# Optimization experiments

Hardware: AMD Instinct MI355X
Metric: run time of the kernel (lower is better)

Reference implementation:

```python
import jax, jax.numpy as jnp
import numpy as np

N, E, IN, H, OUT, K = 50000, 800000, 128, 64, 64, 1024


def setup_inputs() -> dict:
    key = jax.random.key(0)
    ks = jax.random.split(key, 8)
    x = jax.random.normal(ks[0], (N, IN), dtype=jnp.float32)
    edge_index = jax.random.randint(ks[1], (2, E), 0, N, dtype=jnp.int32)
    cluster_id = jax.random.randint(ks[2], (N,), 0, K, dtype=jnp.int32)
    W1 = jax.random.normal(ks[3], (IN, H), dtype=jnp.float32) / np.float32(np.sqrt(IN))
    b1 = jnp.zeros((H,), jnp.float32)
    W2 = jax.random.normal(ks[4], (H, OUT), dtype=jnp.float32) / np.float32(np.sqrt(H))
    b2 = jnp.zeros((OUT,), jnp.float32)
    W_skip = jax.random.normal(ks[5], (H, OUT), dtype=jnp.float32) / np.float32(np.sqrt(H))
    b_skip = jnp.zeros((OUT,), jnp.float32)
    alpha = jnp.full((1,), 1.5, jnp.float32)
    return dict(x=x, edge_index=edge_index, cluster_id=cluster_id, W1=W1, b1=b1,
                W2=W2, b2=b2, W_skip=W_skip, b_skip=b_skip, alpha=alpha)


def gcn_conv_sparse(x, src, dst, n, W, b):
    # PyG GCNConv: transform, then D^{-1/2}(A+I)D^{-1/2} aggregation, then bias.
    h = x @ W  # [n, F_out]
    deg = jax.ops.segment_sum(jnp.ones_like(src, dtype=h.dtype), dst, num_segments=n) + 1.0
    dinv = jax.lax.rsqrt(deg)
    norm = dinv[src] * dinv[dst]  # [E]
    agg = jax.ops.segment_sum(h[src] * norm[:, None], dst, num_segments=n)
    agg = agg + (dinv * dinv)[:, None] * h  # self-loop term
    return agg + b


def reference(x, edge_index, cluster_id, W1, b1, W2, b2, W_skip, b_skip, alpha):
    src, dst = edge_index[0], edge_index[1]
    # conv1 + ReLU (dropout is identity in eval mode)
    x1 = jax.nn.relu(gcn_conv_sparse(x, src, dst, N, W1, b1))  # [N, H]

    # pool_by_partition: scatter-mean node features into K clusters
    sums = jax.ops.segment_sum(x1, cluster_id, num_segments=K)  # [K, H]
    counts = jnp.maximum(jax.ops.segment_sum(jnp.ones((N,), x1.dtype), cluster_id, num_segments=K), 1.0)
    x_p = sums / counts[:, None]

    # deduped pooled edges, self-loops removed == dense 0/1 adjacency with zero diag (K small)
    cu, cv = cluster_id[src], cluster_id[dst]
    A = jnp.zeros((K, K), x1.dtype).at[cu, cv].set(1.0)
    A = A * (1.0 - jnp.eye(K, dtype=x1.dtype))
    A_hat = A + jnp.eye(K, dtype=x1.dtype)
    deg_p = jnp.sum(A_hat, axis=0)  # in-degree at target (PyG computes deg on col)
    dinv_p = jax.lax.rsqrt(deg_p)
    A_norm = dinv_p[:, None] * A_hat * dinv_p[None, :]  # [src, dst]
    h_p = x_p @ W2
    x_p2 = jnp.einsum('st,sf->tf', A_norm, h_p) + b2  # [K, OUT]

    # gather-broadcast + strengthened skip head
    up = x_p2[cluster_id]  # [N, OUT]
    skip = x1 @ W_skip + b_skip
    logits = up + jax.nn.relu(alpha)[0] * skip
    return logits
```

## Files before the change

kernel.cpp:

```cpp
#include <hip/hip_runtime.h>

#define NN 50000
#define NE 800000
#define FIN 128
#define FH 64
#define FOUT 64
#define KC 1024
#define CAP 64
#define EPB 2048
#define NCH ((NE + EPB - 1) / EPB)
#define NBK ((NN + 255) / 256)
#define BCAP 4608

typedef unsigned char  u8;
typedef unsigned short u16;
typedef unsigned int   u32;


__global__ __launch_bounds__(256) void k_part(const int* __restrict__ src,
                                              const int* __restrict__ dst,
                                              const int* __restrict__ cid,
                                              int* __restrict__ gcur,
                                              u32* __restrict__ bin,
                                              u8* __restrict__ AT) {
    __shared__ int hist[256], off[256], cur[256], gbase[256];
    __shared__ u32 sorted[EPB];
    int t = threadIdx.x;
    hist[t] = 0; cur[t] = 0;
    __syncthreads();
    int e0 = blockIdx.x * EPB, e1 = min(NE, e0 + EPB);
    for (int e = e0 + t; e < e1; e += 256)
        atomicAdd(&hist[dst[e] >> 8], 1);
    __syncthreads();
    int v = hist[t];
    off[t] = v;
    __syncthreads();
    for (int o = 1; o < 256; o <<= 1) {
        int u = (t >= o) ? off[t - o] : 0;
        __syncthreads();
        off[t] += u;
        __syncthreads();
    }
    int ex = off[t] - v;
    __syncthreads();
    off[t] = ex;
    __syncthreads();
    for (int e = e0 + t; e < e1; e += 256) {
        int d = dst[e], s = src[e];
        int b = d >> 8, local = d & 255;
        int cu = cid[s], cv = cid[d];
        if (cu != cv) AT[(size_t)cv * KC + cu] = 1;
        int p = off[b] + atomicAdd(&cur[b], 1);
        sorted[p] = ((u32)b << 24) | ((u32)local << 16) | (u32)s;
    }
    __syncthreads();
    if (t < NBK && hist[t]) gbase[t] = atomicAdd(&gcur[t], hist[t]);
    __syncthreads();
    int cnt = e1 - e0;
    for (int i = t; i < cnt; i += 256) {
        u32 e = sorted[i];
        int b = e >> 24;
        int idx = gbase[b] + (i - off[b]);
        if (idx < BCAP) bin[(size_t)b * BCAP + idx] = e;
    }
}

__global__ __launch_bounds__(256) void k_slots(const int* __restrict__ gcur,
                                               const u32* __restrict__ bin,
                                               const int* __restrict__ cid,
                                               int* __restrict__ deg,
                                               float* __restrict__ dinv,
                                               int* __restrict__ counts,
                                               u16* __restrict__ slots) {
    __shared__ u16 sbuf[256 * CAP];
    __shared__ int c_lds[256];
    int t = threadIdx.x, b = blockIdx.x;
    c_lds[t] = 0;
    __syncthreads();
    int cnt = min(gcur[b], BCAP);
    const u32* bp = bin + (size_t)b * BCAP;
    for (int i = t; i < cnt; i += 256) {
        u32 e = bp[i];
        int local = (e >> 16) & 255;
        int pos = atomicAdd(&c_lds[local], 1);
        if (pos < CAP) sbuf[local * CAP + pos] = (u16)(e & 0xffffu);
    }
    __syncthreads();
    int node = b * 256 + t;
    if (node < NN) {
        int d = c_lds[t];
        deg[node] = d;
        dinv[node] = rsqrtf((float)d + 1.0f);
        atomicAdd(&counts[cid[node]], 1);
    }
    int rows = min(256, NN - b * 256);
    int n4 = rows * (CAP * 2 / 16);
    const uint4* sb4 = (const uint4*)sbuf;
    uint4* gs4 = (uint4*)(slots + (size_t)b * 256 * CAP);
    for (int j = t; j < n4; j += 256) gs4[j] = sb4[j];
}

__global__ __launch_bounds__(256) void k_gemm1(const float* __restrict__ x,
                                               const float* __restrict__ W1,
                                               const float* __restrict__ dinv,
                                               float* __restrict__ h) {
    __shared__ float Ws[FIN * FH];
    __shared__ float Xs[32 * FIN];
    int t = threadIdx.x;
    int row_base = blockIdx.x * 32;
    for (int i = t; i < FIN * FH; i += 256) Ws[i] = W1[i];
    {
        const float4* x4 = (const float4*)x;
        float4* xs4 = (float4*)Xs;
        for (int i = t; i < 32 * 32; i += 256) {
            int r = i >> 5, k4 = i & 31;
            int row = row_base + r;
            float4 v = make_float4(0.f, 0.f, 0.f, 0.f);
            if (row < NN) v = x4[(size_t)row * 32 + k4];
            xs4[i] = v;
        }
    }
    __syncthreads();
    int col = t & 31, grp = t >> 5;
    int r0 = grp * 4;
    const float4* p0 = (const float4*)&Xs[(r0 + 0) * FIN];
    const float4* p1 = (const float4*)&Xs[(r0 + 1) * FIN];
    const float4* p2 = (const float4*)&Xs[(r0 + 2) * FIN];
    const float4* p3 = (const float4*)&Xs[(r0 + 3) * FIN];
    float acc00 = 0.f, acc01 = 0.f, acc10 = 0.f, acc11 = 0.f;
    float acc20 = 0.f, acc21 = 0.f, acc30 = 0.f, acc31 = 0.f;
#pragma unroll 2
    for (int k4 = 0; k4 < FIN / 4; ++k4) {
        float4 a0 = p0[k4], a1 = p1[k4], a2 = p2[k4], a3 = p3[k4];
        const float* wp = &Ws[(k4 * 4) * FH + col];
        float w00 = wp[0],          w01 = wp[32];
        float w10 = wp[FH],         w11 = wp[FH + 32];
        float w20 = wp[2 * FH],     w21 = wp[2 * FH + 32];
        float w30 = wp[3 * FH],     w31 = wp[3 * FH + 32];
        acc00 = fmaf(a0.x, w00, fmaf(a0.y, w10, fmaf(a0.z, w20, fmaf(a0.w, w30, acc00))));
        acc01 = fmaf(a0.x, w01, fmaf(a0.y, w11, fmaf(a0.z, w21, fmaf(a0.w, w31, acc01))));
        acc10 = fmaf(a1.x, w00, fmaf(a1.y, w10, fmaf(a1.z, w20, fmaf(a1.w, w30, acc10))));
        acc11 = fmaf(a1.x, w01, fmaf(a1.y, w11, fmaf(a1.z, w21, fmaf(a1.w, w31, acc11))));
        acc20 = fmaf(a2.x, w00, fmaf(a2.y, w10, fmaf(a2.z, w20, fmaf(a2.w, w30, acc20))));
        acc21 = fmaf(a2.x, w01, fmaf(a2.y, w11, fmaf(a2.z, w21, fmaf(a2.w, w31, acc21))));
        acc30 = fmaf(a3.x, w00, fmaf(a3.y, w10, fmaf(a3.z, w20, fmaf(a3.w, w30, acc30))));
        acc31 = fmaf(a3.x, w01, fmaf(a3.y, w11, fmaf(a3.z, w21, fmaf(a3.w, w31, acc31))));
    }
    int row0 = row_base + r0;
    if (row0 + 0 < NN) { float di = dinv[row0 + 0]; h[(size_t)(row0 + 0) * FH + col] = di * acc00; h[(size_t)(row0 + 0) * FH + col + 32] = di * acc01; }
    if (row0 + 1 < NN) { float di = dinv[row0 + 1]; h[(size_t)(row0 + 1) * FH + col] = di * acc10; h[(size_t)(row0 + 1) * FH + col + 32] = di * acc11; }
    if (row0 + 2 < NN) { float di = dinv[row0 + 2]; h[(size_t)(row0 + 2) * FH + col] = di * acc20; h[(size_t)(row0 + 2) * FH + col + 32] = di * acc21; }
    if (row0 + 3 < NN) { float di = dinv[row0 + 3]; h[(size_t)(row0 + 3) * FH + col] = di * acc30; h[(size_t)(row0 + 3) * FH + col + 32] = di * acc31; }
}

__global__ __launch_bounds__(256) void k_gather(const int* __restrict__ deg,
                                                const u16* __restrict__ slots,
                                                const float* __restrict__ dinv,
                                                const float* __restrict__ h,
                                                const float* __restrict__ b1,
                                                const int* __restrict__ cid,
                                                float* __restrict__ x1,
                                                float* __restrict__ sums) {
    int lane = threadIdx.x & 63;
    int node = blockIdx.x * 4 + (threadIdx.x >> 6);
    if (node >= NN) return;
    int q = lane >> 4, fl = lane & 15;
    const float4* h4 = (const float4*)h;
    int cnt = min(deg[node], CAP);
    const u16* cp = slots + (size_t)node * CAP;
    float4 acc = make_float4(0.f, 0.f, 0.f, 0.f);
    {
        int s = (lane < cnt) ? (int)cp[lane] : 0;
        int nFull = cnt >> 2;
        for (int j = 0; j < nFull; ++j) {
            int ss = __shfl(s, j * 4 + q);
            float4 hv = h4[(size_t)ss * 16 + fl];
            acc.x += hv.x; acc.y += hv.y; acc.z += hv.z; acc.w += hv.w;
        }
        int tail = cnt & 3;
        if (tail) {
            int ss = __shfl(s, nFull * 4 + q);
            float m = (q < tail) ? 1.f : 0.f;
            float4 hv = h4[(size_t)ss * 16 + fl];
            acc.x = fmaf(m, hv.x, acc.x);
            acc.y = fmaf(m, hv.y, acc.y);
            acc.z = fmaf(m, hv.z, acc.z);
            acc.w = fmaf(m, hv.w, acc.w);
        }
    }
    acc.x += __shfl_xor(acc.x, 16); acc.y += __shfl_xor(acc.y, 16);
    acc.z += __shfl_xor(acc.z, 16); acc.w += __shfl_xor(acc.w, 16);
    acc.x += __shfl_xor(acc.x, 32); acc.y += __shfl_xor(acc.y, 32);
    acc.z += __shfl_xor(acc.z, 32); acc.w += __shfl_xor(acc.w, 32);
    float di = dinv[node];
    float4 hs = h4[(size_t)node * 16 + fl];
    const float4* b14 = (const float4*)b1;
    float4 bb = b14[fl];
    float4 v;
    v.x = fmaxf(fmaf(di, acc.x + hs.x, bb.x), 0.f);
    v.y = fmaxf(fmaf(di, acc.y + hs.y, bb.y), 0.f);
    v.z = fmaxf(fmaf(di, acc.z + hs.z, bb.z), 0.f);
    v.w = fmaxf(fmaf(di, acc.w + hs.w, bb.w), 0.f);
    if (q == 0) ((float4*)x1)[(size_t)node * 16 + fl] = v;
    int c = cid[node];
    float comp = (q == 0) ? v.x : (q == 1) ? v.y : (q == 2) ? v.z : v.w;
    unsafeAtomicAdd(&sums[(size_t)c * FH + fl * 4 + q], comp);
}

__global__ __launch_bounds__(64) void k_pool(const float* __restrict__ sums,
                                             const int* __restrict__ counts,
                                             const float* __restrict__ W2,
                                             const u8* __restrict__ AT,
                                             float* __restrict__ dinvp,
                                             float* __restrict__ g) {
    __shared__ float xp[FH];
    int s = blockIdx.x, f = threadIdx.x;
    const u32* row = (const u32*)(AT + (size_t)s * KC);
    int pc = __popc(row[f]) + __popc(row[f + 64]) + __popc(row[f + 128]) + __popc(row[f + 192]);
    for (int o = 32; o; o >>= 1) pc += __shfl_xor(pc, o);
    float dp = rsqrtf(1.0f + (float)pc);
    if (f == 0) dinvp[s] = dp;
    float cnt = fmaxf((float)counts[s], 1.0f);
    xp[f] = sums[(size_t)s * FH + f] / cnt;
    __syncthreads();
    float acc = 0.f;
    for (int j = 0; j < FH; ++j) acc = fmaf(xp[j], W2[j * FH + f], acc);
    g[(size_t)s * FH + f] = dp * acc;
}

__global__ __launch_bounds__(256) void k_xp2(const u8* __restrict__ AT,
                                             const float* __restrict__ g,
                                             const float* __restrict__ dinvp,
                                             const float* __restrict__ b2,
                                             float* __restrict__ xp2) {
    __shared__ float4 sm4[4][16];
    int t = blockIdx.x;
    int lane = threadIdx.x & 63, w = threadIdx.x >> 6;
    int q = lane >> 4, fl = lane & 15;
    const u32* roww = (const u32*)(AT + (size_t)t * KC);
    const float4* g4 = (const float4*)g;
    float4 acc = make_float4(0.f, 0.f, 0.f, 0.f);
    int wb = w * 64;
    u32 wv = roww[wb + lane];
    for (int j = 0; j < 16; ++j) {
        u32 word = __shfl((int)wv, j * 4 + q);
        int sidx = (wb + j * 4 + q) * 4;
#pragma unroll
        for (int b = 0; b < 4; ++b) {
            float a = (float)((word >> (8 * b)) & 255u);
            float4 gv = g4[(size_t)(sidx + b) * 16 + fl];
            acc.x = fmaf(a, gv.x, acc.x);
            acc.y = fmaf(a, gv.y, acc.y);
            acc.z = fmaf(a, gv.z, acc.z);
            acc.w = fmaf(a, gv.w, acc.w);
        }
    }
    acc.x += __shfl_xor(acc.x, 16); acc.y += __shfl_xor(acc.y, 16);
    acc.z += __shfl_xor(acc.z, 16); acc.w += __shfl_xor(acc.w, 16);
    acc.x += __shfl_xor(acc.x, 32); acc.y += __shfl_xor(acc.y, 32);
    acc.z += __shfl_xor(acc.z, 32); acc.w += __shfl_xor(acc.w, 32);
    if (q == 0) sm4[w][fl] = acc;
    __syncthreads();
    if (threadIdx.x < 16) {
        int f = threadIdx.x;
        float4 a0 = sm4[0][f], a1 = sm4[1][f], a2 = sm4[2][f], a3 = sm4[3][f];
        float4 gs = g4[(size_t)t * 16 + f];
        float dp = dinvp[t];
        const float4* b24 = (const float4*)b2;
        float4 bb = b24[f];
        float4 o;
        o.x = fmaf(dp, a0.x + a1.x + a2.x + a3.x + gs.x, bb.x);
        o.y = fmaf(dp, a0.y + a1.y + a2.y + a3.y + gs.y, bb.y);
        o.z = fmaf(dp, a0.z + a1.z + a2.z + a3.z + gs.z, bb.z);
        o.w = fmaf(dp, a0.w + a1.w + a2.w + a3.w + gs.w, bb.w);
        ((float4*)xp2)[(size_t)t * 16 + f] = o;
    }
}

__global__ __launch_bounds__(256) void k_final(const float* __restrict__ x1,
                                               const float* __restrict__ Wsk,
                                               const float* __restrict__ bsk,
                                               const float* __restrict__ xp2,
                                               const int* __restrict__ cid,
                                               const float* __restrict__ alpha,
                                               float* __restrict__ out) {
    __shared__ float Ws[FH * FOUT];
    __shared__ float Xs[32 * FH];
    int t = threadIdx.x;
    int row_base = blockIdx.x * 32;
    for (int i = t; i < FH * FOUT; i += 256) Ws[i] = Wsk[i];
    {
        const float4* x4 = (const float4*)x1;
        float4* xs4 = (float4*)Xs;
        for (int i = t; i < 32 * 16; i += 256) {
            int r = i >> 4, k4 = i & 15;
            int row = row_base + r;
            float4 v = make_float4(0.f, 0.f, 0.f, 0.f);
            if (row < NN) v = x4[(size_t)row * 16 + k4];
            xs4[i] = v;
        }
    }
    __syncthreads();
    float al = fmaxf(alpha[0], 0.f);
    int col = t & 31, grp = t >> 5;
    int r0 = grp * 4;
    const float4* p0 = (const float4*)&Xs[(r0 + 0) * FH];
    const float4* p1 = (const float4*)&Xs[(r0 + 1) * FH];
    const float4* p2 = (const float4*)&Xs[(r0 + 2) * FH];
    const float4* p3 = (const float4*)&Xs[(r0 + 3) * FH];
    float acc00 = 0.f, acc01 = 0.f, acc10 = 0.f, acc11 = 0.f;
    float acc20 = 0.f, acc21 = 0.f, acc30 = 0.f, acc31 = 0.f;
#pragma unroll 2
    for (int k4 = 0; k4 < FH / 4; ++k4) {
        float4 a0 = p0[k4], a1 = p1[k4], a2 = p2[k4], a3 = p3[k4];
        const float* wp = &Ws[(k4 * 4) * FOUT + col];
        float w00 = wp[0],           w01 = wp[32];
        float w10 = wp[FOUT],        w11 = wp[FOUT + 32];
        float w20 = wp[2 * FOUT],    w21 = wp[2 * FOUT + 32];
        float w30 = wp[3 * FOUT],    w31 = wp[3 * FOUT + 32];
        acc00 = fmaf(a0.x, w00, fmaf(a0.y, w10, fmaf(a0.z, w20, fmaf(a0.w, w30, acc00))));
        acc01 = fmaf(a0.x, w01, fmaf(a0.y, w11, fmaf(a0.z, w21, fmaf(a0.w, w31, acc01))));
        acc10 = fmaf(a1.x, w00, fmaf(a1.y, w10, fmaf(a1.z, w20, fmaf(a1.w, w30, acc10))));
        acc11 = fmaf(a1.x, w01, fmaf(a1.y, w11, fmaf(a1.z, w21, fmaf(a1.w, w31, acc11))));
        acc20 = fmaf(a2.x, w00, fmaf(a2.y, w10, fmaf(a2.z, w20, fmaf(a2.w, w30, acc20))));
        acc21 = fmaf(a2.x, w01, fmaf(a2.y, w11, fmaf(a2.z, w21, fmaf(a2.w, w31, acc21))));
        acc30 = fmaf(a3.x, w00, fmaf(a3.y, w10, fmaf(a3.z, w20, fmaf(a3.w, w30, acc30))));
        acc31 = fmaf(a3.x, w01, fmaf(a3.y, w11, fmaf(a3.z, w21, fmaf(a3.w, w31, acc31))));
    }
    float bb0 = bsk[col], bb1 = bsk[col + 32];
    int row0 = row_base + r0;
#pragma unroll
    for (int i = 0; i < 4; ++i) {
        float a0 = (i == 0) ? acc00 : (i == 1) ? acc10 : (i == 2) ? acc20 : acc30;
        float a1 = (i == 0) ? acc01 : (i == 1) ? acc11 : (i == 2) ? acc21 : acc31;
        int row = row0 + i;
        if (row < NN) {
            int c = cid[row];
            out[(size_t)row * FOUT + col]      = xp2[(size_t)c * FOUT + col]      + al * (a0 + bb0);
            out[(size_t)row * FOUT + col + 32] = xp2[(size_t)c * FOUT + col + 32] + al * (a1 + bb1);
        }
    }
}

extern "C" void kernel_launch(void* const* d_in, const int* in_sizes, int n_in,
                              void* d_out, int out_size, void* d_ws, size_t ws_size,
                              hipStream_t stream) {
    const float* x    = (const float*)d_in[0];
    const int*   ei   = (const int*)d_in[1];
    const int*   cid  = (const int*)d_in[2];
    const float* W1   = (const float*)d_in[3];
    const float* b1   = (const float*)d_in[4];
    const float* W2   = (const float*)d_in[5];
    const float* b2   = (const float*)d_in[6];
    const float* Wsk  = (const float*)d_in[7];
    const float* bsk  = (const float*)d_in[8];
    const float* alpha= (const float*)d_in[9];
    float* out = (float*)d_out;
    const int* src = ei;
    const int* dst = ei + NE;

    char* ws = (char*)d_ws;
    size_t cur = 0;
    auto alloc = [&](size_t nb) { cur = (cur + 255) & ~(size_t)255; size_t o = cur; cur += nb; return o; };
    size_t o_sums = alloc((size_t)KC * FH * 4);
    size_t o_AT   = alloc((size_t)KC * KC);
    size_t o_cnt  = alloc((size_t)KC * 4);
    size_t o_gcur = alloc((size_t)NBK * 4);
    size_t zero_bytes = cur;
    size_t o_bin  = alloc((size_t)NBK * BCAP * 4);
    size_t o_slot = alloc((size_t)NN * CAP * 2);
    size_t o_deg  = alloc((size_t)NN * 4);
    size_t o_x1   = alloc((size_t)NN * FH * 4);
    size_t o_h    = alloc((size_t)NN * FH * 4);
    size_t o_dinv = alloc((size_t)NN * 4);
    size_t o_g    = alloc((size_t)KC * FH * 4);
    size_t o_xp2  = alloc((size_t)KC * FH * 4);
    size_t o_dinvp= alloc((size_t)KC * 4);
    (void)ws_size; (void)in_sizes; (void)n_in; (void)out_size;

    float* sums = (float*)(ws + o_sums);
    u8*    AT   = (u8*)(ws + o_AT);
    int*   cnt  = (int*)(ws + o_cnt);
    int*   gcur = (int*)(ws + o_gcur);
    u32*   bin  = (u32*)(ws + o_bin);
    u16*   slot = (u16*)(ws + o_slot);
    int*   deg  = (int*)(ws + o_deg);
    float* x1   = (float*)(ws + o_x1);
    float* h    = (float*)(ws + o_h);
    float* dinv = (float*)(ws + o_dinv);
    float* g    = (float*)(ws + o_g);
    float* xp2  = (float*)(ws + o_xp2);
    float* dinvp= (float*)(ws + o_dinvp);

    hipMemsetAsync(d_ws, 0, zero_bytes, stream);

    const int NRB = (NN + 31) / 32;
    k_part  <<<NCH, 256, 0, stream>>>(src, dst, cid, gcur, bin, AT);
    k_slots <<<NBK, 256, 0, stream>>>(gcur, bin, cid, deg, dinv, cnt, slot);
    k_gemm1 <<<NRB, 256, 0, stream>>>(x, W1, dinv, h);
    k_gather<<<(NN + 3) / 4, 256, 0, stream>>>(deg, slot, dinv, h, b1, cid, x1, sums);
    k_pool  <<<KC, 64, 0, stream>>>(sums, cnt, W2, AT, dinvp, g);
    k_xp2   <<<KC, 256, 0, stream>>>(AT, g, dinvp, b2, xp2);
    k_final <<<NRB, 256, 0, stream>>>(x1, Wsk, bsk, xp2, cid, alpha, out);
}
```

Measured before the change: 212.5 us.

## Store intermediate node features in fp16 and cache edges in LDS during partitioning

The transformed features h, written by the first GEMM and gathered per edge, are now stored as half precision, which halves the bytes moved by the random neighbor gather. The GEMM output layout changes so each thread writes adjacent column pairs as half2. Separately, the partition kernel reads each edge's src/dst and cluster ids once, keeps the packed edge in LDS, and reuses it for the local sort instead of reloading from global memory. The fp16 storage adds rounding error to the aggregated features.

```diff
diff --git a/kernel.cpp b/kernel.cpp
--- a/kernel.cpp
+++ b/kernel.cpp
@@ -1,4 +1,5 @@
 #include <hip/hip_runtime.h>
+#include <hip/hip_fp16.h>
 
 #define NN 50000
 #define NE 800000
@@ -16,7 +17,6 @@
 typedef unsigned short u16;
 typedef unsigned int   u32;
 
-
 __global__ __launch_bounds__(256) void k_part(const int* __restrict__ src,
                                               const int* __restrict__ dst,
                                               const int* __restrict__ cid,
@@ -24,13 +24,21 @@
                                               u32* __restrict__ bin,
                                               u8* __restrict__ AT) {
     __shared__ int hist[256], off[256], cur[256], gbase[256];
+    __shared__ u32 raw[EPB];
     __shared__ u32 sorted[EPB];
     int t = threadIdx.x;
     hist[t] = 0; cur[t] = 0;
     __syncthreads();
     int e0 = blockIdx.x * EPB, e1 = min(NE, e0 + EPB);
-    for (int e = e0 + t; e < e1; e += 256)
-        atomicAdd(&hist[dst[e] >> 8], 1);
+    int cnt = e1 - e0;
+    for (int e = e0 + t; e < e1; e += 256) {
+        int d = dst[e], s = src[e];
+        int b = d >> 8, local = d & 255;
+        int cu = cid[s], cv = cid[d];
+        if (cu != cv) AT[(size_t)cv * KC + cu] = 1;
+        atomicAdd(&hist[b], 1);
+        raw[e - e0] = ((u32)b << 24) | ((u32)local << 16) | (u32)s;
+    }
     __syncthreads();
     int v = hist[t];
     off[t] = v;
@@ -45,18 +53,15 @@
     __syncthreads();
     off[t] = ex;
     __syncthreads();
-    for (int e = e0 + t; e < e1; e += 256) {
-        int d = dst[e], s = src[e];
-        int b = d >> 8, local = d & 255;
-        int cu = cid[s], cv = cid[d];
-        if (cu != cv) AT[(size_t)cv * KC + cu] = 1;
+    for (int i = t; i < cnt; i += 256) {
+        u32 e = raw[i];
+        int b = e >> 24;
         int p = off[b] + atomicAdd(&cur[b], 1);
-        sorted[p] = ((u32)b << 24) | ((u32)local << 16) | (u32)s;
+        sorted[p] = e;
     }
     __syncthreads();
     if (t < NBK && hist[t]) gbase[t] = atomicAdd(&gcur[t], hist[t]);
     __syncthreads();
-    int cnt = e1 - e0;
     for (int i = t; i < cnt; i += 256) {
         u32 e = sorted[i];
         int b = e >> 24;
@@ -103,7 +108,7 @@
 __global__ __launch_bounds__(256) void k_gemm1(const float* __restrict__ x,
                                                const float* __restrict__ W1,
                                                const float* __restrict__ dinv,
-                                               float* __restrict__ h) {
+                                               __half* __restrict__ h) {
     __shared__ float Ws[FIN * FH];
     __shared__ float Xs[32 * FIN];
     int t = threadIdx.x;
@@ -121,7 +126,8 @@
         }
     }
     __syncthreads();
-    int col = t & 31, grp = t >> 5;
+    int c = t & 31, grp = t >> 5;
+    int colp = c * 2;
     int r0 = grp * 4;
     const float4* p0 = (const float4*)&Xs[(r0 + 0) * FIN];
     const float4* p1 = (const float4*)&Xs[(r0 + 1) * FIN];
@@ -132,31 +138,32 @@
 #pragma unroll 2
     for (int k4 = 0; k4 < FIN / 4; ++k4) {
         float4 a0 = p0[k4], a1 = p1[k4], a2 = p2[k4], a3 = p3[k4];
-        const float* wp = &Ws[(k4 * 4) * FH + col];
-        float w00 = wp[0],          w01 = wp[32];
-        float w10 = wp[FH],         w11 = wp[FH + 32];
-        float w20 = wp[2 * FH],     w21 = wp[2 * FH + 32];
-        float w30 = wp[3 * FH],     w31 = wp[3 * FH + 32];
-        acc00 = fmaf(a0.x, w00, fmaf(a0.y, w10, fmaf(a0.z, w20, fmaf(a0.w, w30, acc00))));
-        acc01 = fmaf(a0.x, w01, fmaf(a0.y, w11, fmaf(a0.z, w21, fmaf(a0.w, w31, acc01))));
-        acc10 = fmaf(a1.x, w00, fmaf(a1.y, w10, fmaf(a1.z, w20, fmaf(a1.w, w30, acc10))));
-        acc11 = fmaf(a1.x, w01, fmaf(a1.y, w11, fmaf(a1.z, w21, fmaf(a1.w, w31, acc11))));
-        acc20 = fmaf(a2.x, w00, fmaf(a2.y, w10, fmaf(a2.z, w20, fmaf(a2.w, w30, acc20))));
-        acc21 = fmaf(a2.x, w01, fmaf(a2.y, w11, fmaf(a2.z, w21, fmaf(a2.w, w31, acc21))));
-        acc30 = fmaf(a3.x, w00, fmaf(a3.y, w10, fmaf(a3.z, w20, fmaf(a3.w, w30, acc30))));
-        acc31 = fmaf(a3.x, w01, fmaf(a3.y, w11, fmaf(a3.z, w21, fmaf(a3.w, w31, acc31))));
-    }
+        const float* wb = &Ws[(k4 * 4) * FH + colp];
+        float2 w0 = *(const float2*)&wb[0];
+        float2 w1 = *(const float2*)&wb[FH];
+        float2 w2 = *(const float2*)&wb[2 * FH];
+        float2 w3 = *(const float2*)&wb[3 * FH];
+        acc00 = fmaf(a0.x, w0.x, fmaf(a0.y, w1.x, fmaf(a0.z, w2.x, fmaf(a0.w, w3.x, acc00))));
+        acc01 = fmaf(a0.x, w0.y, fmaf(a0.y, w1.y, fmaf(a0.z, w2.y, fmaf(a0.w, w3.y, acc01))));
+        acc10 = fmaf(a1.x, w0.x, fmaf(a1.y, w1.x, fmaf(a1.z, w2.x, fmaf(a1.w, w3.x, acc10))));
+        acc11 = fmaf(a1.x, w0.y, fmaf(a1.y, w1.y, fmaf(a1.z, w2.y, fmaf(a1.w, w3.y, acc11))));
+        acc20 = fmaf(a2.x, w0.x, fmaf(a2.y, w1.x, fmaf(a2.z, w2.x, fmaf(a2.w, w3.x, acc20))));
+        acc21 = fmaf(a2.x, w0.y, fmaf(a2.y, w1.y, fmaf(a2.z, w2.y, fmaf(a2.w, w3.y, acc21))));
+        acc30 = fmaf(a3.x, w0.x, fmaf(a3.y, w1.x, fmaf(a3.z, w2.x, fmaf(a3.w, w3.x, acc30))));
+        acc31 = fmaf(a3.x, w0.y, fmaf(a3.y, w1.y, fmaf(a3.z, w2.y, fmaf(a3.w, w3.y, acc31))));
+    }
+    __half2* h2 = (__half2*)h;
     int row0 = row_base + r0;
-    if (row0 + 0 < NN) { float di = dinv[row0 + 0]; h[(size_t)(row0 + 0) * FH + col] = di * acc00; h[(size_t)(row0 + 0) * FH + col + 32] = di * acc01; }
-    if (row0 + 1 < NN) { float di = dinv[row0 + 1]; h[(size_t)(row0 + 1) * FH + col] = di * acc10; h[(size_t)(row0 + 1) * FH + col + 32] = di * acc11; }
-    if (row0 + 2 < NN) { float di = dinv[row0 + 2]; h[(size_t)(row0 + 2) * FH + col] = di * acc20; h[(size_t)(row0 + 2) * FH + col + 32] = di * acc21; }
-    if (row0 + 3 < NN) { float di = dinv[row0 + 3]; h[(size_t)(row0 + 3) * FH + col] = di * acc30; h[(size_t)(row0 + 3) * FH + col + 32] = di * acc31; }
+    if (row0 + 0 < NN) { float di = dinv[row0 + 0]; h2[(size_t)(row0 + 0) * 32 + c] = __floats2half2_rn(di * acc00, di * acc01); }
+    if (row0 + 1 < NN) { float di = dinv[row0 + 1]; h2[(size_t)(row0 + 1) * 32 + c] = __floats2half2_rn(di * acc10, di * acc11); }
+    if (row0 + 2 < NN) { float di = dinv[row0 + 2]; h2[(size_t)(row0 + 2) * 32 + c] = __floats2half2_rn(di * acc20, di * acc21); }
+    if (row0 + 3 < NN) { float di = dinv[row0 + 3]; h2[(size_t)(row0 + 3) * 32 + c] = __floats2half2_rn(di * acc30, di * acc31); }
 }
 
 __global__ __launch_bounds__(256) void k_gather(const int* __restrict__ deg,
                                                 const u16* __restrict__ slots,
                                                 const float* __restrict__ dinv,
-                                                const float* __restrict__ h,
+                                                const __half* __restrict__ h,
                                                 const float* __restrict__ b1,
                                                 const int* __restrict__ cid,
                                                 float* __restrict__ x1,
@@ -165,7 +172,7 @@
     int node = blockIdx.x * 4 + (threadIdx.x >> 6);
     if (node >= NN) return;
     int q = lane >> 4, fl = lane & 15;
-    const float4* h4 = (const float4*)h;
+    const float2* h2 = (const float2*)h;
     int cnt = min(deg[node], CAP);
     const u16* cp = slots + (size_t)node * CAP;
     float4 acc = make_float4(0.f, 0.f, 0.f, 0.f);
@@ -174,18 +181,22 @@
         int nFull = cnt >> 2;
         for (int j = 0; j < nFull; ++j) {
             int ss = __shfl(s, j * 4 + q);
-            float4 hv = h4[(size_t)ss * 16 + fl];
-            acc.x += hv.x; acc.y += hv.y; acc.z += hv.z; acc.w += hv.w;
+            float2 rawv = h2[(size_t)ss * 16 + fl];
+            float2 f0 = __half22float2(*(__half2*)&rawv.x);
+            float2 f1 = __half22float2(*(__half2*)&rawv.y);
+            acc.x += f0.x; acc.y += f0.y; acc.z += f1.x; acc.w += f1.y;
         }
         int tail = cnt & 3;
         if (tail) {
             int ss = __shfl(s, nFull * 4 + q);
             float m = (q < tail) ? 1.f : 0.f;
-            float4 hv = h4[(size_t)ss * 16 + fl];
-            acc.x = fmaf(m, hv.x, acc.x);
-            acc.y = fmaf(m, hv.y, acc.y);
-            acc.z = fmaf(m, hv.z, acc.z);
-            acc.w = fmaf(m, hv.w, acc.w);
+            float2 rawv = h2[(size_t)ss * 16 + fl];
+            float2 f0 = __half22float2(*(__half2*)&rawv.x);
+            float2 f1 = __half22float2(*(__half2*)&rawv.y);
+            acc.x = fmaf(m, f0.x, acc.x);
+            acc.y = fmaf(m, f0.y, acc.y);
+            acc.z = fmaf(m, f1.x, acc.z);
+            acc.w = fmaf(m, f1.y, acc.w);
         }
     }
     acc.x += __shfl_xor(acc.x, 16); acc.y += __shfl_xor(acc.y, 16);
@@ -193,14 +204,16 @@
     acc.x += __shfl_xor(acc.x, 32); acc.y += __shfl_xor(acc.y, 32);
     acc.z += __shfl_xor(acc.z, 32); acc.w += __shfl_xor(acc.w, 32);
     float di = dinv[node];
-    float4 hs = h4[(size_t)node * 16 + fl];
+    float2 rawv = h2[(size_t)node * 16 + fl];
+    float2 hs0 = __half22float2(*(__half2*)&rawv.x);
+    float2 hs1 = __half22float2(*(__half2*)&rawv.y);
     const float4* b14 = (const float4*)b1;
     float4 bb = b14[fl];
     float4 v;
-    v.x = fmaxf(fmaf(di, acc.x + hs.x, bb.x), 0.f);
-    v.y = fmaxf(fmaf(di, acc.y + hs.y, bb.y), 0.f);
-    v.z = fmaxf(fmaf(di, acc.z + hs.z, bb.z), 0.f);
-    v.w = fmaxf(fmaf(di, acc.w + hs.w, bb.w), 0.f);
+    v.x = fmaxf(fmaf(di, acc.x + hs0.x, bb.x), 0.f);
+    v.y = fmaxf(fmaf(di, acc.y + hs0.y, bb.y), 0.f);
+    v.z = fmaxf(fmaf(di, acc.z + hs1.x, bb.z), 0.f);
+    v.w = fmaxf(fmaf(di, acc.w + hs1.y, bb.w), 0.f);
     if (q == 0) ((float4*)x1)[(size_t)node * 16 + fl] = v;
     int c = cid[node];
     float comp = (q == 0) ? v.x : (q == 1) ? v.y : (q == 2) ? v.z : v.w;
@@ -371,7 +384,7 @@
     size_t o_slot = alloc((size_t)NN * CAP * 2);
     size_t o_deg  = alloc((size_t)NN * 4);
     size_t o_x1   = alloc((size_t)NN * FH * 4);
-    size_t o_h    = alloc((size_t)NN * FH * 4);
+    size_t o_h    = alloc((size_t)NN * FH * 2);
     size_t o_dinv = alloc((size_t)NN * 4);
     size_t o_g    = alloc((size_t)KC * FH * 4);
     size_t o_xp2  = alloc((size_t)KC * FH * 4);
@@ -386,7 +399,7 @@
     u16*   slot = (u16*)(ws + o_slot);
     int*   deg  = (int*)(ws + o_deg);
     float* x1   = (float*)(ws + o_x1);
-    float* h    = (float*)(ws + o_h);
+    __half* h   = (__half*)(ws + o_h);
     float* dinv = (float*)(ws + o_dinv);
     float* g    = (float*)(ws + o_g);
     float* xp2  = (float*)(ws + o_xp2);
```

New measurement: 203.6 us. 4.2% less time.
